# Kernel optimization log

Hardware: AMD Instinct MI355X
Metric: run time of the kernel (lower is better)

The kernel has to match this reference:

```python
import jax, jax.numpy as jnp
import numpy as np

N = 65536      # number of points
D = 3          # spatial dimension (init arg 'dimension')
C = 64         # feature channels
K = 16         # neighbors returned by faiss knn search
BLOCK = 512    # query block size for chunked brute-force distances
GRID = 128     # spatial_size


def setup_inputs() -> dict:
    key = jax.random.key(0)
    k1, k2 = jax.random.split(key)
    coords = jax.random.randint(k1, (N, D), 0, GRID, dtype=jnp.int32)
    features = jax.random.normal(k2, (N, C), dtype=jnp.float32)
    return {"coords": coords, "features": features}


def reference(coords, features):
    """Brute-force KNN over integer point coords (faiss-equivalent exact L2
    search), then sparse input-layer construction: for each point, gather the
    features of its K nearest neighbors and sum them (SCN InputLayer mode=3)."""
    cf = coords.astype(jnp.float32)                 # [N, D]
    db_sq = jnp.sum(cf * cf, axis=1)                # [N]

    n_blocks = N // BLOCK
    queries = cf.reshape(n_blocks, BLOCK, D)

    def step(_, q):                                 # q: [BLOCK, D]
        q_sq = jnp.sum(q * q, axis=1)               # [BLOCK]
        # squared L2 distances to all database points: [BLOCK, N]
        dist = q_sq[:, None] - 2.0 * (q @ cf.T) + db_sq[None, :]
        _, idx = jax.lax.top_k(-dist, K)            # [BLOCK, K] nearest indices
        nb = features[idx]                          # irregular gather [BLOCK, K, C]
        return None, jnp.sum(nb, axis=1)            # mode=3: sum duplicates/neighbors

    _, out = jax.lax.scan(step, None, queries)      # [n_blocks, BLOCK, C]
    return out.reshape(N, C)
```

## Files before the change

### kernel.cpp

```cpp
#include <hip/hip_runtime.h>


typedef unsigned int uint;
typedef unsigned short ushort;
typedef short short2v __attribute__((ext_vector_type(2)));

#define NPTS   65536
#define NCELL  32768

static __device__ inline short2v u2s(uint v) { union { uint u; short2v s; } c; c.u = v; return c.s; }
static __device__ inline uint s2u(short2v v) { union { uint u; short2v s; } c; c.s = v; return c.u; }

static __device__ inline int dot2acc(short2v a, short2v b, int c) {
#if __has_builtin(__builtin_amdgcn_sdot2)
    return __builtin_amdgcn_sdot2(a, b, c, false);
#else
    return (int)a.x * (int)b.x + (int)a.y * (int)b.y + c;
#endif
}

__global__ __launch_bounds__(256) void cell_count(const int* __restrict__ coords,
                                                  uint* __restrict__ counts) {
    int i = blockIdx.x * 256 + threadIdx.x;
    int x = coords[3 * i + 0], y = coords[3 * i + 1], z = coords[3 * i + 2];
    int cell = (x >> 2) | ((y >> 2) << 5) | ((z >> 2) << 10);
    atomicAdd(&counts[cell], 1u);
}

__global__ __launch_bounds__(256) void scan_chunk(const uint* __restrict__ counts,
                                                  uint* __restrict__ gcur,
                                                  uint* __restrict__ starts,
                                                  uint* __restrict__ ends,
                                                  uint* __restrict__ cursors) {
    __shared__ uint wsum[4];
    __shared__ uint sbase;
    int tid = threadIdx.x;
    int lane = tid & 63, wv = tid >> 6;
    int cell = blockIdx.x * 256 + tid;
    uint c = counts[cell];
    uint v = c;
#pragma unroll
    for (int off = 1; off < 64; off <<= 1) {
        uint u = __shfl_up(v, off, 64);
        if (lane >= off) v += u;
    }
    if (lane == 63) wsum[wv] = v;
    __syncthreads();
    if (tid == 0)
        sbase = atomicAdd(gcur, wsum[0] + wsum[1] + wsum[2] + wsum[3]);
    __syncthreads();
    uint woff = 0;
#pragma unroll
    for (int j = 0; j < 4; ++j) woff += (j < wv) ? wsum[j] : 0u;
    uint st = sbase + woff + v - c;
    starts[cell]  = st;
    ends[cell]    = st + c;
    cursors[cell] = st;
}

__global__ __launch_bounds__(256) void cell_scatter(const int* __restrict__ coords,
                                                    uint* __restrict__ cursors,
                                                    uint2* __restrict__ sorted) {
    int i = blockIdx.x * 256 + threadIdx.x;
    int x = coords[3 * i + 0], y = coords[3 * i + 1], z = coords[3 * i + 2];
    int cell = (x >> 2) | ((y >> 2) << 5) | ((z >> 2) << 10);
    uint pos = atomicAdd(&cursors[cell], 1u);
    sorted[pos] = make_uint2((uint)(x | (y << 16)), (uint)(i | (z << 16)));
}

__global__ __launch_bounds__(256, 8) void knn_search(const uint* __restrict__ starts,
                                                     const uint* __restrict__ ends,
                                                     const uint2* __restrict__ sorted,
                                                     const float* __restrict__ feat,
                                                     float* __restrict__ out) {
    int blk  = (blockIdx.x & 7) * 256 + (blockIdx.x >> 3);
    int wave = threadIdx.x >> 6;
    int lane = threadIdx.x & 63;
    int qslot = lane & 7;
    int slice = lane >> 3;
    int qpos = blk * 32 + wave * 8 + qslot;

    uint2 me = sorted[qpos];
    uint qxy = me.x;
    uint qzp = me.y & 0xFFFF0000u;
    uint qidx = me.y & 0xFFFFu;
    int qx = (int)(me.x & 0xFFFFu);
    int qy = (int)(me.x >> 16);
    int qz = (int)(me.y >> 16);
    int cx = qx >> 2, cy = qy >> 2, cz = qz >> 2;

    uint k[16];
#pragma unroll
    for (int j = 0; j < 16; ++j) k[j] = 0xFFFFFFFFu;

    auto insert1 = [&](uint2 pt) {
        short2v A = u2s(pt.x) - u2s(qxy);
        short2v B = u2s(pt.y) - u2s(qzp);
        uint Bu = s2u(B);
        short2v Bm = u2s(Bu & 0xFFFF0000u);
        int d2 = dot2acc(A, A, dot2acc(Bm, Bm, 0));
        uint key = ((uint)d2 << 16) + (Bu & 0xFFFFu);
#pragma unroll
        for (int j = 15; j >= 1; --j)
            asm("v_med3_u32 %0, %1, %2, %3"
                : "=v"(k[j]) : "v"(k[j - 1]), "v"(k[j]), "v"(key));
        k[0] = min(k[0], key);
    };

    auto scan8 = [&](uint p0, uint p1) {
        for (uint p = p0 + (uint)slice; p < p1; p += 8u) insert1(sorted[p]);
    };

    auto merge_min = [&](int mask) {
        uint b[16];
#pragma unroll
        for (int j = 0; j < 16; ++j) b[j] = __shfl_xor(k[j], mask, 64);
#pragma unroll
        for (int j = 0; j < 16; ++j) k[j] = min(k[j], b[15 - j]);
    };
    auto clean = [&]() {
#pragma unroll
        for (int d = 8; d >= 1; d >>= 1) {
#pragma unroll
            for (int i = 0; i < 16; ++i) {
                if ((i & d) == 0) {
                    uint lo = min(k[i], k[i + d]);
                    uint hi = max(k[i], k[i + d]);
                    k[i] = lo;
                    k[i + d] = hi;
                }
            }
        }
    };
    auto merge = [&](int mask) { merge_min(mask); clean(); };
    auto merge_all = [&]() { merge(8); merge(16); merge(32); };

    int xa = min(max(cx - ((qx & 3) < 2 ? 2 : 1), 0), 28);
    int ya = min(max(cy - ((qy & 3) < 2 ? 2 : 1), 0), 28);
    int za = min(max(cz - ((qz & 3) < 2 ? 2 : 1), 0), 28);

    {
        int rbA = ((ya + (slice & 3)) << 5) | ((za + (slice >> 2)) << 10);
        int rbB = ((ya + (slice & 3)) << 5) | ((za + 2 + (slice >> 2)) << 10);
        uint pA = starts[rbA + xa], eA = ends[rbA + xa + 3];
        uint pB = starts[rbB + xa], eB = ends[rbB + xa + 3];
        while (__any((pA < eA) || (pB < eB))) {
            bool a0 = pA < eA, a1 = pA + 1 < eA;
            bool b0 = pB < eB, b1 = pB + 1 < eB;
            uint2 A0, A1, B0, B1;
            if (a0) A0 = sorted[pA];
            if (a1) A1 = sorted[pA + 1];
            if (b0) B0 = sorted[pB];
            if (b1) B1 = sorted[pB + 1];
            pA += (a0 ? 1u : 0u) + (a1 ? 1u : 0u);
            pB += (b0 ? 1u : 0u) + (b1 ? 1u : 0u);
            if (a0) insert1(A0);
            if (b0) insert1(B0);
            if (a1) insert1(A1);
            if (b1) insert1(B1);
        }
    }
    merge(8); merge(16); merge_min(32);
    uint mx = k[0];
#pragma unroll
    for (int j = 1; j < 16; ++j) mx = max(mx, k[j]);

    bool redo = (mx >> 16) >= 49u;
    if (__any(redo)) {
        clean();
        if (redo || slice != 0) {
#pragma unroll
            for (int j = 0; j < 16; ++j) k[j] = 0xFFFFFFFFu;
        }
        if (redo) {
            int xl = max(cx - 2, 0), xh = min(cx + 2, 31);
            int yl = max(cy - 2, 0), yh = min(cy + 2, 31);
            int zl = max(cz - 2, 0), zh = min(cz + 2, 31);
            for (int z = zl; z <= zh; ++z)
                for (int y = yl; y <= yh; ++y) {
                    int rb = (y << 5) | (z << 10);
                    scan8(starts[rb + xl], ends[rb + xh]);
                }
        }
        merge_all();
        for (int r = 3; r < 32; ++r) {
            uint b = (uint)(4 * r - 3);
            bool active = (k[15] >> 16) >= b * b;
            if (!__any(active)) break;
            if (slice != 0) {
#pragma unroll
                for (int j = 0; j < 16; ++j) k[j] = 0xFFFFFFFFu;
            }
            if (active) {
                int z0 = cz - r < 0 ? 0 : cz - r;
                int z1 = cz + r > 31 ? 31 : cz + r;
                for (int z = z0; z <= z1; ++z) {
                    bool zface = (z == cz - r) || (z == cz + r);
                    int y0 = cy - r < 0 ? 0 : cy - r;
                    int y1 = cy + r > 31 ? 31 : cy + r;
                    for (int y = y0; y <= y1; ++y) {
                        bool face = zface || (y == cy - r) || (y == cy + r);
                        int rb = (y << 5) | (z << 10);
                        if (face) {
                            int x0 = cx - r < 0 ? 0 : cx - r;
                            int x1 = cx + r > 31 ? 31 : cx + r;
                            scan8(starts[rb + x0], ends[rb + x1]);
                        } else {
                            int xL = cx - r;
                            if (xL >= 0) scan8(starts[rb + xL], ends[rb + xL]);
                            int xR = cx + r;
                            if (xR <= 31) scan8(starts[rb + xR], ends[rb + xR]);
                        }
                    }
                }
            }
            merge_all();
        }
    }

    uint ki[16];
#pragma unroll
    for (int j = 0; j < 16; ++j) ki[j] = k[j] & 0xFFFFu;

    int ch = lane & 15;
    int qg = lane >> 4;
#pragma unroll
    for (int p = 0; p < 2; ++p) {
        int qs = p * 4 + qg;
        uint qorig = __shfl(qidx, qs, 64);
        float4 acc = make_float4(0.f, 0.f, 0.f, 0.f);
#pragma unroll
        for (int j = 0; j < 16; ++j) {
            uint nj = __shfl(ki[j], qs, 64);
            float4 v = reinterpret_cast<const float4*>(feat)[nj * 16u + (uint)ch];
            acc.x += v.x; acc.y += v.y; acc.z += v.z; acc.w += v.w;
        }
        reinterpret_cast<float4*>(out)[qorig * 16u + (uint)ch] = acc;
    }
}

extern "C" void kernel_launch(void* const* d_in, const int* in_sizes, int n_in,
                              void* d_out, int out_size, void* d_ws, size_t ws_size,
                              hipStream_t stream) {
    const int*   coords = (const int*)d_in[0];
    const float* feat   = (const float*)d_in[1];
    float*       out    = (float*)d_out;

    uint* W = (uint*)d_ws;
    uint*  gcur    = W;
    uint*  counts  = W + 8;
    uint*  starts  = W + 32776;
    uint*  ends    = W + 65544;
    uint*  cursors = W + 98312;
    uint2* sorted  = (uint2*)(W + 131080);

    hipMemsetAsync(W, 0, (8 + NCELL) * sizeof(uint), stream);
    cell_count<<<NPTS / 256, 256, 0, stream>>>(coords, counts);
    scan_chunk<<<NCELL / 256, 256, 0, stream>>>(counts, gcur, starts, ends, cursors);
    cell_scatter<<<NPTS / 256, 256, 0, stream>>>(coords, cursors, sorted);
    knn_search<<<2048, 256, 0, stream>>>(starts, ends, sorted, feat, out);
}
```

Baseline: 61.50 us.

## Pack 16 queries per wave with 4 slices and drop the ends array

The search kernel now handles 16 queries per wave with 4 lane slices instead of 8 queries with 8 slices. Each slice walks 4 z-rows of the initial 4x4x4 cell box, so one merge stage is removed, and the grid is halved with launch bounds relaxed to 4 waves per SIMD. The ends array is replaced by reading starts[cell+1]. To make that valid, chunk offsets are now computed from per-chunk totals gathered by an extra atomic in cell_count, rather than by an ordered atomic on a global cursor. The risks are more atomic contention on the 128 chunk counters, higher register pressure, and less parallelism per query.

```diff
diff --git a/kernel.cpp b/kernel.cpp
--- a/kernel.cpp
+++ b/kernel.cpp
@@ -20,23 +20,32 @@
 }
 
 __global__ __launch_bounds__(256) void cell_count(const int* __restrict__ coords,
-                                                  uint* __restrict__ counts) {
+                                                  uint* __restrict__ counts,
+                                                  uint* __restrict__ chunktot) {
     int i = blockIdx.x * 256 + threadIdx.x;
     int x = coords[3 * i + 0], y = coords[3 * i + 1], z = coords[3 * i + 2];
     int cell = (x >> 2) | ((y >> 2) << 5) | ((z >> 2) << 10);
     atomicAdd(&counts[cell], 1u);
+    atomicAdd(&chunktot[cell >> 8], 1u);
 }
 
 __global__ __launch_bounds__(256) void scan_chunk(const uint* __restrict__ counts,
-                                                  uint* __restrict__ gcur,
+                                                  const uint* __restrict__ chunktot,
                                                   uint* __restrict__ starts,
-                                                  uint* __restrict__ ends,
                                                   uint* __restrict__ cursors) {
     __shared__ uint wsum[4];
-    __shared__ uint sbase;
+    int b = blockIdx.x;
     int tid = threadIdx.x;
     int lane = tid & 63, wv = tid >> 6;
-    int cell = blockIdx.x * 256 + tid;
+    int cell = b * 256 + tid;
+
+    uint t0 = chunktot[lane];
+    uint t1 = chunktot[64 + lane];
+    uint s = (lane < b ? t0 : 0u) + (64 + lane < b ? t1 : 0u);
+#pragma unroll
+    for (int off = 32; off; off >>= 1) s += __shfl_xor(s, off, 64);
+    uint base = s;
+
     uint c = counts[cell];
     uint v = c;
 #pragma unroll
@@ -46,16 +55,13 @@
     }
     if (lane == 63) wsum[wv] = v;
     __syncthreads();
-    if (tid == 0)
-        sbase = atomicAdd(gcur, wsum[0] + wsum[1] + wsum[2] + wsum[3]);
-    __syncthreads();
     uint woff = 0;
 #pragma unroll
     for (int j = 0; j < 4; ++j) woff += (j < wv) ? wsum[j] : 0u;
-    uint st = sbase + woff + v - c;
+    uint st = base + woff + v - c;
     starts[cell]  = st;
-    ends[cell]    = st + c;
     cursors[cell] = st;
+    if (cell == NCELL - 1) starts[NCELL] = st + c;
 }
 
 __global__ __launch_bounds__(256) void cell_scatter(const int* __restrict__ coords,
@@ -68,17 +74,16 @@
     sorted[pos] = make_uint2((uint)(x | (y << 16)), (uint)(i | (z << 16)));
 }
 
-__global__ __launch_bounds__(256, 8) void knn_search(const uint* __restrict__ starts,
-                                                     const uint* __restrict__ ends,
+__global__ __launch_bounds__(256, 4) void knn_search(const uint* __restrict__ starts,
                                                      const uint2* __restrict__ sorted,
                                                      const float* __restrict__ feat,
                                                      float* __restrict__ out) {
-    int blk  = (blockIdx.x & 7) * 256 + (blockIdx.x >> 3);
+    int blk  = (blockIdx.x & 7) * 128 + (blockIdx.x >> 3);
     int wave = threadIdx.x >> 6;
     int lane = threadIdx.x & 63;
-    int qslot = lane & 7;
-    int slice = lane >> 3;
-    int qpos = blk * 32 + wave * 8 + qslot;
+    int qslot = lane & 15;
+    int slice = lane >> 4;
+    int qpos = blk * 64 + wave * 16 + qslot;
 
     uint2 me = sorted[qpos];
     uint qxy = me.x;
@@ -107,8 +112,8 @@
         k[0] = min(k[0], key);
     };
 
-    auto scan8 = [&](uint p0, uint p1) {
-        for (uint p = p0 + (uint)slice; p < p1; p += 8u) insert1(sorted[p]);
+    auto scan4 = [&](uint p0, uint p1) {
+        for (uint p = p0 + (uint)slice; p < p1; p += 4u) insert1(sorted[p]);
     };
 
     auto merge_min = [&](int mask) {
@@ -133,34 +138,51 @@
         }
     };
     auto merge = [&](int mask) { merge_min(mask); clean(); };
-    auto merge_all = [&]() { merge(8); merge(16); merge(32); };
+    auto merge_all = [&]() { merge(16); merge(32); };
 
     int xa = min(max(cx - ((qx & 3) < 2 ? 2 : 1), 0), 28);
     int ya = min(max(cy - ((qy & 3) < 2 ? 2 : 1), 0), 28);
     int za = min(max(cz - ((qz & 3) < 2 ? 2 : 1), 0), 28);
 
     {
-        int rbA = ((ya + (slice & 3)) << 5) | ((za + (slice >> 2)) << 10);
-        int rbB = ((ya + (slice & 3)) << 5) | ((za + 2 + (slice >> 2)) << 10);
-        uint pA = starts[rbA + xa], eA = ends[rbA + xa + 3];
-        uint pB = starts[rbB + xa], eB = ends[rbB + xa + 3];
-        while (__any((pA < eA) || (pB < eB))) {
+        int ybase = (ya + slice) << 5;
+        int rb0 = ybase | ((za + 0) << 10);
+        int rb1 = ybase | ((za + 1) << 10);
+        int rb2 = ybase | ((za + 2) << 10);
+        int rb3 = ybase | ((za + 3) << 10);
+        uint pA = starts[rb0 + xa], eA = starts[rb0 + xa + 4];
+        uint pB = starts[rb1 + xa], eB = starts[rb1 + xa + 4];
+        uint pC = starts[rb2 + xa], eC = starts[rb2 + xa + 4];
+        uint pD = starts[rb3 + xa], eD = starts[rb3 + xa + 4];
+        while (__any((pA < eA) || (pB < eB) || (pC < eC) || (pD < eD))) {
             bool a0 = pA < eA, a1 = pA + 1 < eA;
             bool b0 = pB < eB, b1 = pB + 1 < eB;
-            uint2 A0, A1, B0, B1;
+            bool c0 = pC < eC, c1 = pC + 1 < eC;
+            bool d0 = pD < eD, d1 = pD + 1 < eD;
+            uint2 A0, A1, B0, B1, C0, C1, D0, D1;
             if (a0) A0 = sorted[pA];
             if (a1) A1 = sorted[pA + 1];
             if (b0) B0 = sorted[pB];
             if (b1) B1 = sorted[pB + 1];
+            if (c0) C0 = sorted[pC];
+            if (c1) C1 = sorted[pC + 1];
+            if (d0) D0 = sorted[pD];
+            if (d1) D1 = sorted[pD + 1];
             pA += (a0 ? 1u : 0u) + (a1 ? 1u : 0u);
             pB += (b0 ? 1u : 0u) + (b1 ? 1u : 0u);
+            pC += (c0 ? 1u : 0u) + (c1 ? 1u : 0u);
+            pD += (d0 ? 1u : 0u) + (d1 ? 1u : 0u);
             if (a0) insert1(A0);
             if (b0) insert1(B0);
+            if (c0) insert1(C0);
+            if (d0) insert1(D0);
             if (a1) insert1(A1);
             if (b1) insert1(B1);
-        }
-    }
-    merge(8); merge(16); merge_min(32);
+            if (c1) insert1(C1);
+            if (d1) insert1(D1);
+        }
+    }
+    merge(16); merge_min(32);
     uint mx = k[0];
 #pragma unroll
     for (int j = 1; j < 16; ++j) mx = max(mx, k[j]);
@@ -179,7 +201,7 @@
             for (int z = zl; z <= zh; ++z)
                 for (int y = yl; y <= yh; ++y) {
                     int rb = (y << 5) | (z << 10);
-                    scan8(starts[rb + xl], ends[rb + xh]);
+                    scan4(starts[rb + xl], starts[rb + xh + 1]);
                 }
         }
         merge_all();
@@ -204,12 +226,12 @@
                         if (face) {
                             int x0 = cx - r < 0 ? 0 : cx - r;
                             int x1 = cx + r > 31 ? 31 : cx + r;
-                            scan8(starts[rb + x0], ends[rb + x1]);
+                            scan4(starts[rb + x0], starts[rb + x1 + 1]);
                         } else {
                             int xL = cx - r;
-                            if (xL >= 0) scan8(starts[rb + xL], ends[rb + xL]);
+                            if (xL >= 0) scan4(starts[rb + xL], starts[rb + xL + 1]);
                             int xR = cx + r;
-                            if (xR <= 31) scan8(starts[rb + xR], ends[rb + xR]);
+                            if (xR <= 31) scan4(starts[rb + xR], starts[rb + xR + 1]);
                         }
                     }
                 }
@@ -225,7 +247,7 @@
     int ch = lane & 15;
     int qg = lane >> 4;
 #pragma unroll
-    for (int p = 0; p < 2; ++p) {
+    for (int p = 0; p < 4; ++p) {
         int qs = p * 4 + qg;
         uint qorig = __shfl(qidx, qs, 64);
         float4 acc = make_float4(0.f, 0.f, 0.f, 0.f);
@@ -247,16 +269,15 @@
     float*       out    = (float*)d_out;
 
     uint* W = (uint*)d_ws;
-    uint*  gcur    = W;
-    uint*  counts  = W + 8;
-    uint*  starts  = W + 32776;
-    uint*  ends    = W + 65544;
-    uint*  cursors = W + 98312;
-    uint2* sorted  = (uint2*)(W + 131080);
-
-    hipMemsetAsync(W, 0, (8 + NCELL) * sizeof(uint), stream);
-    cell_count<<<NPTS / 256, 256, 0, stream>>>(coords, counts);
-    scan_chunk<<<NCELL / 256, 256, 0, stream>>>(counts, gcur, starts, ends, cursors);
+    uint*  chunktot = W;
+    uint*  counts   = W + 128;
+    uint*  starts   = W + 32896;
+    uint*  cursors  = W + 65668;
+    uint2* sorted   = (uint2*)(W + 98436);
+
+    hipMemsetAsync(W, 0, (128 + NCELL) * sizeof(uint), stream);
+    cell_count<<<NPTS / 256, 256, 0, stream>>>(coords, counts, chunktot);
+    scan_chunk<<<NCELL / 256, 256, 0, stream>>>(counts, chunktot, starts, cursors);
     cell_scatter<<<NPTS / 256, 256, 0, stream>>>(coords, cursors, sorted);
-    knn_search<<<2048, 256, 0, stream>>>(starts, ends, sorted, feat, out);
-}
+    knn_search<<<1024, 256, 0, stream>>>(starts, sorted, feat, out);
+}
```

New measurement: 112.0 us. 1.82x slower.
